# Performance work log

Hardware: AMD Instinct MI355X
Metric: run time of the kernel (lower is better)

## Reference

```python
import jax, jax.numpy as jnp
import numpy as np

# R2D2-style NghSampler2 config
NGH, SUBQ, SUBD, POS_D, NEG_D, BORDER, SUBD_NEG = 7, 8, 1, 3, 5, 16, 8

def _make_offsets():
    rad = (NGH // SUBD) * NGH
    pos, neg = [], []
    for j in range(-rad, rad + 1, SUBD):
        for i in range(-rad, rad + 1, SUBD):
            d2 = i * i + j * j
            if d2 <= POS_D ** 2:
                pos.append((i, j))
            elif NEG_D ** 2 <= d2 <= NGH ** 2:
                neg.append((i, j))
    # rows: [x(i), y(j)], matching torch .view(-1,2).t()
    return np.array(pos, np.int32).T, np.array(neg, np.int32).T

POS_OFF, NEG_OFF = _make_offsets()  # [2,29], [2,80]

def _grid(B, H, W, step):
    xs = np.arange(BORDER, W - BORDER, step)
    ys = np.arange(BORDER, H - BORDER, step)
    H1, W1 = len(ys), len(xs)
    b1 = np.repeat(np.arange(B), H1 * W1)
    y1 = np.tile(np.repeat(ys, W1), B)
    x1 = np.tile(np.tile(xs, H1), B)
    return b1, y1, x1, (B, H1, W1)

def setup_inputs() -> dict:
    key = jax.random.key(0)
    k1, k2, k3, k4, k5 = jax.random.split(key, 5)
    B, C, H, W = 4, 128, 256, 256
    feat1 = jax.random.normal(k1, (B, C, H, W), jnp.float32)
    feat2 = jax.random.normal(k2, (B, C, H, W), jnp.float32)
    conf1 = jax.random.uniform(k3, (B, 1, H, W), jnp.float32)
    conf2 = jax.random.uniform(k4, (B, 1, H, W), jnp.float32)
    aflow = jax.random.uniform(k5, (B, 2, H, W), jnp.float32) * (W - 1)
    return {"feat1": feat1, "feat2": feat2, "conf1": conf1, "conf2": conf2, "aflow": aflow}

def reference(feat1, feat2, conf1, conf2, aflow):
    B, C, H, W = feat1.shape
    b1n, y1n, x1n, shape = _grid(B, H, W, SUBQ)
    b1, y1, x1 = jnp.asarray(b1n), jnp.asarray(y1n), jnp.asarray(x1n)
    pos_off, neg_off = jnp.asarray(POS_OFF), jnp.asarray(NEG_OFF)

    f1 = feat1[b1, :, y1, x1]                      # [Q,C] query descriptors
    qconf = conf1[b1, 0, y1, x1].reshape(shape)    # [B,H1,W1]
    xy2 = (aflow[b1, :, y1, x1] + 0.5).astype(jnp.int32).T  # [2,Q] (x,y)
    mask = ((xy2[0] >= 0) & (xy2[1] >= 0) & (xy2[0] < W) & (xy2[1] < H)).reshape(shape)

    def clamp(xy):
        return jnp.stack([jnp.clip(xy[0], 0, W - 1), jnp.clip(xy[1], 0, H - 1)])

    # positives: gather feat2 at GT-correspondence + pos offsets, dot with f1
    xy2p = clamp(xy2[:, None, :] + pos_off[:, :, None])      # [2,P,Q]
    f2p = feat2[b1, :, xy2p[1], xy2p[0]]                     # [P,Q,C]
    ps_all = jnp.einsum('qc,pqc->qp', f1, f2p)               # [Q,P]
    pscores = ps_all.max(axis=1, keepdims=True)              # [Q,1]
    pos = jnp.argmax(ps_all, axis=1)                         # [Q]
    sel = clamp(xy2 + pos_off[:, pos])                       # [2,Q]
    qconf = (qconf + conf2[b1, 0, sel[1], sel[0]].reshape(shape)) / 2

    # negatives: ring of offsets around GT correspondence
    xy2n = clamp(xy2[:, None, :] + neg_off[:, :, None])      # [2,N,Q]
    f2n = feat2[b1, :, xy2n[1], xy2n[0]]                     # [N,Q,C]
    nscores = jnp.einsum('qc,nqc->qn', f1, f2n)              # [Q,N]

    # distractors on a regular grid in image 2
    b3n, y3n, x3n, _ = _grid(B, H, W, SUBD_NEG)
    b3, y3, x3 = jnp.asarray(b3n), jnp.asarray(y3n), jnp.asarray(x3n)
    distractors = feat2[b3, :, y3, x3]                       # [Q2,C]
    dscores = f1 @ distractors.T                             # [Q,Q2]
    dis2 = (x3[None, :] - xy2[0][:, None]) ** 2 \
         + (y3[None, :] - xy2[1][:, None]) ** 2 \
         + (b3[None, :] != b1[:, None]).astype(jnp.int32) * NEG_D ** 2
    dscores = jnp.where(dis2 < NEG_D ** 2, 0.0, dscores)

    scores = jnp.concatenate([pscores, nscores, dscores], axis=1)
    npos = pscores.shape[1]
    gt = jnp.concatenate([
        jnp.ones((scores.shape[0], npos), jnp.uint8),
        jnp.zeros((scores.shape[0], scores.shape[1] - npos), jnp.uint8)], axis=1)
    return scores, gt, mask, qconf
```

## Files before the change

### kernel.cpp

```cpp
#include <hip/hip_runtime.h>

#define CCH   128
#define HH    256
#define WW    256
#define BB    4
#define H1    28
#define W1    28
#define QTOT  3136
#define NPOS  29
#define NNEG  80
#define NDIS  3136
#define SCOLS 3217

typedef short s8v __attribute__((ext_vector_type(8)));
typedef float f4v __attribute__((ext_vector_type(4)));

__device__ __forceinline__ unsigned short f2bf(float f) {
  unsigned int u = __float_as_uint(f);
  u += 0x7fffu + ((u >> 16) & 1u);
  return (unsigned short)(u >> 16);
}
__device__ __forceinline__ float bf2f(unsigned short h) {
  return __uint_as_float(((unsigned int)h) << 16);
}

__constant__ int POS_I[NPOS] = {
  0, -2,-1,0,1,2, -2,-1,0,1,2, -3,-2,-1,0,1,2,3, -2,-1,0,1,2, -2,-1,0,1,2, 0};
__constant__ int POS_J[NPOS] = {
  -3, -2,-2,-2,-2,-2, -1,-1,-1,-1,-1, 0,0,0,0,0,0,0, 1,1,1,1,1, 2,2,2,2,2, 3};
__constant__ int NEG_I[NNEG] = {
  0, -3,-2,-1,0,1,2,3, -4,-3,-2,-1,0,1,2,3,4, -5,-4,-3,3,4,5, -6,-5,-4,4,5,6,
  -6,-5,5,6, -6,-5,5,6, -7,-6,-5,5,6,7, -6,-5,5,6, -6,-5,5,6, -6,-5,-4,4,5,6,
  -5,-4,-3,3,4,5, -4,-3,-2,-1,0,1,2,3,4, -3,-2,-1,0,1,2,3, 0};
__constant__ int NEG_J[NNEG] = {
  -7, -6,-6,-6,-6,-6,-6,-6, -5,-5,-5,-5,-5,-5,-5,-5,-5, -4,-4,-4,-4,-4,-4,
  -3,-3,-3,-3,-3,-3, -2,-2,-2,-2, -1,-1,-1,-1, 0,0,0,0,0,0, 1,1,1,1, 2,2,2,2,
  3,3,3,3,3,3, 4,4,4,4,4,4, 5,5,5,5,5,5,5,5,5, 6,6,6,6,6,6,6, 7};

__global__ void transpose_kernel(const float* __restrict__ feat2,
                                 unsigned short* __restrict__ feat2T) {
  __shared__ unsigned short tile[CCH][33];
  int x0 = blockIdx.x * 32;
  int y  = blockIdx.y;
  int b  = blockIdx.z;
  int tid = threadIdx.x;
  const float* src = feat2 + ((size_t)b * CCH * HH + y) * WW;
  #pragma unroll
  for (int it = 0; it < 16; ++it) {
    int idx = it * 256 + tid;
    int c = idx >> 5, xi = idx & 31;
    tile[c][xi] = f2bf(src[(size_t)c * HH * WW + x0 + xi]);
  }
  __syncthreads();
  int xi = tid >> 3, cg = (tid & 7) * 16;
  __align__(16) unsigned short tmp[16];
  #pragma unroll
  for (int k = 0; k < 16; ++k) tmp[k] = tile[cg + k][xi];
  unsigned short* dst = feat2T + ((size_t)((b * HH + y) * WW) + x0 + xi) * CCH + cg;
  *(uint4*)dst       = *(const uint4*)tmp;
  *(uint4*)(dst + 8) = *(const uint4*)(tmp + 8);
}

__global__ void gather_kernel(const float* __restrict__ feat1,
                              const unsigned short* __restrict__ feat2T,
                              const float* __restrict__ aflow,
                              unsigned short* __restrict__ F1bf,
                              unsigned short* __restrict__ F2bf,
                              int* __restrict__ X2, int* __restrict__ Y2,
                              float* __restrict__ mask_out) {
  int q = blockIdx.x, c = threadIdx.x;
  int b = q / (H1 * W1), r = q % (H1 * W1);
  int y = 16 + 8 * (r / W1);
  int x = 16 + 8 * (r % W1);
  F1bf[(size_t)q * CCH + c] = f2bf(feat1[((size_t)(b * CCH + c) * HH + y) * WW + x]);
  F2bf[(size_t)q * CCH + c] = feat2T[((size_t)((b * HH + y) * WW) + x) * CCH + c];
  if (c == 0) {
    float ax = aflow[((size_t)(b * 2 + 0) * HH + y) * WW + x];
    float ay = aflow[((size_t)(b * 2 + 1) * HH + y) * WW + x];
    int x2 = (int)(ax + 0.5f);
    int y2 = (int)(ay + 0.5f);
    X2[q] = x2; Y2[q] = y2;
    mask_out[q] = (x2 >= 0 && y2 >= 0 && x2 < WW && y2 < HH) ? 1.0f : 0.0f;
  }
}

__global__ void posneg_kernel(const unsigned short* __restrict__ feat2T,
                              const float* __restrict__ conf1,
                              const float* __restrict__ conf2,
                              const unsigned short* __restrict__ F1bf,
                              const int* __restrict__ X2, const int* __restrict__ Y2,
                              float* __restrict__ scores, float* __restrict__ gt,
                              float* __restrict__ qconf_out) {
  __shared__ float f1s[CCH];
  __shared__ float ps[NPOS];
  int q = blockIdx.x, t = threadIdx.x;
  int b = q / (H1 * W1), r = q % (H1 * W1);
  int y = 16 + 8 * (r / W1);
  int x = 16 + 8 * (r % W1);
  if (t < CCH) f1s[t] = bf2f(F1bf[(size_t)q * CCH + t]);
  int x2 = X2[q], y2 = Y2[q];
  __syncthreads();

  if (t < 2 * (NPOS + NNEG)) {
    int off = t >> 1, half = t & 1;
    int di = (off < NPOS) ? POS_I[off] : NEG_I[off - NPOS];
    int dj = (off < NPOS) ? POS_J[off] : NEG_J[off - NPOS];
    int xk = min(max(x2 + di, 0), WW - 1);
    int yk = min(max(y2 + dj, 0), HH - 1);
    const uint4* p4 = (const uint4*)(feat2T +
        ((size_t)((b * HH + yk) * WW) + xk) * CCH + half * 64);
    float acc = 0.f;
    #pragma unroll
    for (int i = 0; i < 8; ++i) {
      uint4 v = p4[i];
      const unsigned int vs[4] = {v.x, v.y, v.z, v.w};
      #pragma unroll
      for (int j = 0; j < 4; ++j) {
        int c = half * 64 + i * 8 + j * 2;
        acc += f1s[c]     * __uint_as_float(vs[j] << 16);
        acc += f1s[c + 1] * __uint_as_float(vs[j] & 0xffff0000u);
      }
    }
    acc += __shfl_xor(acc, 1);
    if (half == 0) {
      if (off < NPOS) ps[off] = acc;
      else            scores[(size_t)q * SCOLS + 1 + (off - NPOS)] = acc;
    }
  }
  if (t < 1 + NNEG)
    gt[(size_t)q * SCOLS + t] = (t == 0) ? 1.0f : 0.0f;
  __syncthreads();

  if (t == 0) {
    float best = ps[0]; int bi = 0;
    for (int k = 1; k < NPOS; ++k)
      if (ps[k] > best) { best = ps[k]; bi = k; }
    scores[(size_t)q * SCOLS] = best;
    int sx = min(max(x2 + POS_I[bi], 0), WW - 1);
    int sy = min(max(y2 + POS_J[bi], 0), HH - 1);
    float c1 = conf1[((size_t)b * HH + y) * WW + x];
    float c2 = conf2[((size_t)b * HH + sy) * WW + sx];
    qconf_out[q] = 0.5f * (c1 + c2);
  }
}

__global__ void dscore_kernel(const unsigned short* __restrict__ F1bf,
                              const unsigned short* __restrict__ F2bf,
                              const int* __restrict__ X2, const int* __restrict__ Y2,
                              float* __restrict__ scores, float* __restrict__ gt) {
  int w = threadIdx.x >> 6, lane = threadIdx.x & 63;
  int qb = blockIdx.y * 64 + w * 16;
  int db = blockIdx.x * 64;
  int m  = lane & 15;
  int ko = (lane >> 4) * 8;

  f4v acc[4];
  #pragma unroll
  for (int dt = 0; dt < 4; ++dt) acc[dt] = (f4v){0.f, 0.f, 0.f, 0.f};

  #pragma unroll
  for (int kk = 0; kk < 4; ++kk) {
    s8v a = *(const s8v*)(F1bf + (size_t)(qb + m) * CCH + kk * 32 + ko);
    #pragma unroll
    for (int dt = 0; dt < 4; ++dt) {
      s8v bfr = *(const s8v*)(F2bf + (size_t)(db + dt * 16 + m) * CCH + kk * 32 + ko);
      acc[dt] = __builtin_amdgcn_mfma_f32_16x16x32_bf16(a, bfr, acc[dt], 0, 0, 0);
    }
  }

  int rbase = (lane >> 4) * 4, col = lane & 15;
  int x2v[4], y2v[4], qbat[4];
  #pragma unroll
  for (int r = 0; r < 4; ++r) {
    int q = qb + rbase + r;
    x2v[r] = X2[q]; y2v[r] = Y2[q]; qbat[r] = q / (H1 * W1);
  }
  #pragma unroll
  for (int dt = 0; dt < 4; ++dt) {
    int d = db + dt * 16 + col;
    int dbat = d / (H1 * W1), dr = d % (H1 * W1);
    int dy = 16 + 8 * (dr / W1), dx = 16 + 8 * (dr % W1);
    #pragma unroll
    for (int r = 0; r < 4; ++r) {
      int q = qb + rbase + r;
      int ddx = dx - x2v[r], ddy = dy - y2v[r];
      int dis2 = ddx * ddx + ddy * ddy + (dbat != qbat[r] ? 25 : 0);
      float v = acc[dt][r];
      if (dis2 < 25) v = 0.f;
      size_t o = (size_t)q * SCOLS + 1 + NNEG + d;
      scores[o] = v;
      gt[o] = 0.f;
    }
  }
}

extern "C" void kernel_launch(void* const* d_in, const int* in_sizes, int n_in,
                              void* d_out, int out_size, void* d_ws, size_t ws_size,
                              hipStream_t stream) {
  const float* feat1 = (const float*)d_in[0];
  const float* feat2 = (const float*)d_in[1];
  const float* conf1 = (const float*)d_in[2];
  const float* conf2 = (const float*)d_in[3];
  const float* aflow = (const float*)d_in[4];

  float* out       = (float*)d_out;
  float* scores    = out;
  float* gt        = out + (size_t)QTOT * SCOLS;
  float* mask_out  = out + 2 * (size_t)QTOT * SCOLS;
  float* qconf_out = mask_out + QTOT;

  unsigned short* feat2T = (unsigned short*)d_ws;
  unsigned short* F1bf   = feat2T + (size_t)BB * HH * WW * CCH;
  unsigned short* F2bf   = F1bf + (size_t)QTOT * CCH;
  int* X2 = (int*)(F2bf + (size_t)QTOT * CCH);
  int* Y2 = X2 + QTOT;

  dim3 gT(WW / 32, HH, BB);
  transpose_kernel<<<gT, 256, 0, stream>>>(feat2, feat2T);
  gather_kernel<<<QTOT, CCH, 0, stream>>>(feat1, feat2T, aflow, F1bf, F2bf, X2, Y2, mask_out);
  posneg_kernel<<<QTOT, 256, 0, stream>>>(feat2T, conf1, conf2, F1bf, X2, Y2, scores, gt, qconf_out);
  dim3 gD(NDIS / 64, QTOT / 64);
  dscore_kernel<<<gD, 256, 0, stream>>>(F1bf, F2bf, X2, Y2, scores, gt);
}
```

Baseline: 344.0 us.

## Coalesce dscore stores via LDS tile, bulk-zero gt, wave-per-offset posneg

The dscore kernel now stages MFMA results in a shared-memory tile so each wave writes contiguous 64-float row segments instead of scattered per-lane stores. It also no longer writes gt. A separate vectorized float4 kernel zeroes the whole gt matrix up front, and posneg sets the single 1.0 entry per row. Posneg is restructured so that each wave handles one offset at a time, with lanes covering channels and a full wave reduction, and its score writes are batched through shared memory. The aim is to cut uncoalesced global write traffic, which dominates output, at the cost of an extra launch and an LDS round trip.

```diff
diff --git a/kernel.cpp b/kernel.cpp
--- a/kernel.cpp
+++ b/kernel.cpp
@@ -36,6 +36,11 @@
   -7, -6,-6,-6,-6,-6,-6,-6, -5,-5,-5,-5,-5,-5,-5,-5,-5, -4,-4,-4,-4,-4,-4,
   -3,-3,-3,-3,-3,-3, -2,-2,-2,-2, -1,-1,-1,-1, 0,0,0,0,0,0, 1,1,1,1, 2,2,2,2,
   3,3,3,3,3,3, 4,4,4,4,4,4, 5,5,5,5,5,5,5,5,5, 6,6,6,6,6,6,6, 7};
+
+__global__ void zerogt_kernel(float4* __restrict__ gt4, int n4) {
+  int i = blockIdx.x * blockDim.x + threadIdx.x;
+  if (i < n4) gt4[i] = make_float4(0.f, 0.f, 0.f, 0.f);
+}
 
 __global__ void transpose_kernel(const float* __restrict__ feat2,
                                  unsigned short* __restrict__ feat2T) {
@@ -91,65 +96,64 @@
                               const int* __restrict__ X2, const int* __restrict__ Y2,
                               float* __restrict__ scores, float* __restrict__ gt,
                               float* __restrict__ qconf_out) {
-  __shared__ float f1s[CCH];
-  __shared__ float ps[NPOS];
-  int q = blockIdx.x, t = threadIdx.x;
+  __shared__ float posv[NPOS];
+  __shared__ float negv[NNEG];
+  __shared__ float bestv;
+  int q = blockIdx.x;
+  int t = threadIdx.x;
+  int w = t >> 6, lane = t & 63;
   int b = q / (H1 * W1), r = q % (H1 * W1);
   int y = 16 + 8 * (r / W1);
   int x = 16 + 8 * (r % W1);
-  if (t < CCH) f1s[t] = bf2f(F1bf[(size_t)q * CCH + t]);
+
+  unsigned int f1p = ((const unsigned int*)(F1bf + (size_t)q * CCH))[lane];
+  float f1a = __uint_as_float(f1p << 16);
+  float f1b = __uint_as_float(f1p & 0xffff0000u);
   int x2 = X2[q], y2 = Y2[q];
-  __syncthreads();
-
-  if (t < 2 * (NPOS + NNEG)) {
-    int off = t >> 1, half = t & 1;
+
+  for (int off = w; off < NPOS + NNEG; off += 4) {
     int di = (off < NPOS) ? POS_I[off] : NEG_I[off - NPOS];
     int dj = (off < NPOS) ? POS_J[off] : NEG_J[off - NPOS];
     int xk = min(max(x2 + di, 0), WW - 1);
     int yk = min(max(y2 + dj, 0), HH - 1);
-    const uint4* p4 = (const uint4*)(feat2T +
-        ((size_t)((b * HH + yk) * WW) + xk) * CCH + half * 64);
-    float acc = 0.f;
+    unsigned int v = ((const unsigned int*)(feat2T +
+        ((size_t)((b * HH + yk) * WW) + xk) * CCH))[lane];
+    float s = f1a * __uint_as_float(v << 16)
+            + f1b * __uint_as_float(v & 0xffff0000u);
     #pragma unroll
-    for (int i = 0; i < 8; ++i) {
-      uint4 v = p4[i];
-      const unsigned int vs[4] = {v.x, v.y, v.z, v.w};
-      #pragma unroll
-      for (int j = 0; j < 4; ++j) {
-        int c = half * 64 + i * 8 + j * 2;
-        acc += f1s[c]     * __uint_as_float(vs[j] << 16);
-        acc += f1s[c + 1] * __uint_as_float(vs[j] & 0xffff0000u);
-      }
+    for (int o = 32; o > 0; o >>= 1) s += __shfl_xor(s, o);
+    if (lane == 0) {
+      if (off < NPOS) posv[off] = s;
+      else            negv[off - NPOS] = s;
     }
-    acc += __shfl_xor(acc, 1);
-    if (half == 0) {
-      if (off < NPOS) ps[off] = acc;
-      else            scores[(size_t)q * SCOLS + 1 + (off - NPOS)] = acc;
-    }
-  }
-  if (t < 1 + NNEG)
-    gt[(size_t)q * SCOLS + t] = (t == 0) ? 1.0f : 0.0f;
+  }
   __syncthreads();
 
   if (t == 0) {
-    float best = ps[0]; int bi = 0;
+    float best = posv[0]; int bi = 0;
     for (int k = 1; k < NPOS; ++k)
-      if (ps[k] > best) { best = ps[k]; bi = k; }
-    scores[(size_t)q * SCOLS] = best;
+      if (posv[k] > best) { best = posv[k]; bi = k; }
+    bestv = best;
     int sx = min(max(x2 + POS_I[bi], 0), WW - 1);
     int sy = min(max(y2 + POS_J[bi], 0), HH - 1);
     float c1 = conf1[((size_t)b * HH + y) * WW + x];
     float c2 = conf2[((size_t)b * HH + sy) * WW + sx];
     qconf_out[q] = 0.5f * (c1 + c2);
-  }
+    gt[(size_t)q * SCOLS] = 1.0f;
+  }
+  __syncthreads();
+
+  if (t < 1 + NNEG)
+    scores[(size_t)q * SCOLS + t] = (t == 0) ? bestv : negv[t - 1];
 }
 
 __global__ void dscore_kernel(const unsigned short* __restrict__ F1bf,
                               const unsigned short* __restrict__ F2bf,
                               const int* __restrict__ X2, const int* __restrict__ Y2,
-                              float* __restrict__ scores, float* __restrict__ gt) {
+                              float* __restrict__ scores) {
+  __shared__ float tile[64][66];
   int w = threadIdx.x >> 6, lane = threadIdx.x & 63;
-  int qb = blockIdx.y * 64 + w * 16;
+  int qb = blockIdx.y * 64;
   int db = blockIdx.x * 64;
   int m  = lane & 15;
   int ko = (lane >> 4) * 8;
@@ -160,7 +164,7 @@
 
   #pragma unroll
   for (int kk = 0; kk < 4; ++kk) {
-    s8v a = *(const s8v*)(F1bf + (size_t)(qb + m) * CCH + kk * 32 + ko);
+    s8v a = *(const s8v*)(F1bf + (size_t)(qb + w * 16 + m) * CCH + kk * 32 + ko);
     #pragma unroll
     for (int dt = 0; dt < 4; ++dt) {
       s8v bfr = *(const s8v*)(F2bf + (size_t)(db + dt * 16 + m) * CCH + kk * 32 + ko);
@@ -169,28 +173,28 @@
   }
 
   int rbase = (lane >> 4) * 4, col = lane & 15;
-  int x2v[4], y2v[4], qbat[4];
-  #pragma unroll
-  for (int r = 0; r < 4; ++r) {
-    int q = qb + rbase + r;
-    x2v[r] = X2[q]; y2v[r] = Y2[q]; qbat[r] = q / (H1 * W1);
-  }
-  #pragma unroll
-  for (int dt = 0; dt < 4; ++dt) {
-    int d = db + dt * 16 + col;
-    int dbat = d / (H1 * W1), dr = d % (H1 * W1);
-    int dy = 16 + 8 * (dr / W1), dx = 16 + 8 * (dr % W1);
+  #pragma unroll
+  for (int dt = 0; dt < 4; ++dt)
     #pragma unroll
-    for (int r = 0; r < 4; ++r) {
-      int q = qb + rbase + r;
-      int ddx = dx - x2v[r], ddy = dy - y2v[r];
-      int dis2 = ddx * ddx + ddy * ddy + (dbat != qbat[r] ? 25 : 0);
-      float v = acc[dt][r];
-      if (dis2 < 25) v = 0.f;
-      size_t o = (size_t)q * SCOLS + 1 + NNEG + d;
-      scores[o] = v;
-      gt[o] = 0.f;
-    }
+    for (int r = 0; r < 4; ++r)
+      tile[w * 16 + rbase + r][dt * 16 + col] = acc[dt][r];
+  __syncthreads();
+
+  int d = db + lane;
+  int dbat = d / (H1 * W1), dr = d % (H1 * W1);
+  int dy = 16 + 8 * (dr / W1), dx = 16 + 8 * (dr % W1);
+
+  #pragma unroll
+  for (int i = 0; i < 16; ++i) {
+    int row = w * 16 + i;
+    int q = qb + row;
+    int x2 = X2[q], y2 = Y2[q];
+    int qbat = q / (H1 * W1);
+    int ddx = dx - x2, ddy = dy - y2;
+    int dis2 = ddx * ddx + ddy * ddy + (dbat != qbat ? 25 : 0);
+    float v = tile[row][lane];
+    if (dis2 < 25) v = 0.f;
+    scores[(size_t)q * SCOLS + 1 + NNEG + d] = v;
   }
 }
 
@@ -215,10 +219,12 @@
   int* X2 = (int*)(F2bf + (size_t)QTOT * CCH);
   int* Y2 = X2 + QTOT;
 
+  int n4 = (QTOT * SCOLS) / 4;
+  zerogt_kernel<<<(n4 + 255) / 256, 256, 0, stream>>>((float4*)gt, n4);
   dim3 gT(WW / 32, HH, BB);
   transpose_kernel<<<gT, 256, 0, stream>>>(feat2, feat2T);
   gather_kernel<<<QTOT, CCH, 0, stream>>>(feat1, feat2T, aflow, F1bf, F2bf, X2, Y2, mask_out);
   posneg_kernel<<<QTOT, 256, 0, stream>>>(feat2T, conf1, conf2, F1bf, X2, Y2, scores, gt, qconf_out);
   dim3 gD(NDIS / 64, QTOT / 64);
-  dscore_kernel<<<gD, 256, 0, stream>>>(F1bf, F2bf, X2, Y2, scores, gt);
-}
+  dscore_kernel<<<gD, 256, 0, stream>>>(F1bf, F2bf, X2, Y2, scores);
+}
```

Result: slower. 375.3 us (+9.1%).
